# Optimization experiments

Hardware: AMD Instinct MI355X
Metric: run time of the kernel (lower is better)

The kernel has to match this reference:

```python
import jax, jax.numpy as jnp
import numpy as np

N_EMBD = 2048
N_HEAD = 16
HEAD_DIM = N_EMBD // N_HEAD
BATCH = 2
SEQ = 2048


def setup_inputs() -> dict:
    key = jax.random.key(0)
    k1, k2, k3 = jax.random.split(key, 3)
    scale = 0.02
    return {
        "hidden_states": jax.random.normal(k1, (BATCH, SEQ, N_EMBD), dtype=jnp.float32),
        "c_attn_w": jax.random.normal(k2, (N_EMBD, 3 * N_EMBD), dtype=jnp.float32) * scale,
        "c_attn_b": jnp.zeros((3 * N_EMBD,), dtype=jnp.float32),
        "c_proj_w": jax.random.normal(k3, (N_EMBD, N_EMBD), dtype=jnp.float32) * scale,
        "c_proj_b": jnp.zeros((N_EMBD,), dtype=jnp.float32),
    }


def reference(hidden_states, c_attn_w, c_attn_b, c_proj_w, c_proj_b):
    B, S, E = hidden_states.shape
    # Fused QKV projection (Conv1D: x @ W + b)
    qkv = hidden_states @ c_attn_w + c_attn_b  # [B, S, 3E]
    q, k, v = jnp.split(qkv, 3, axis=-1)
    # split heads -> [B, H, S, D]
    def split_heads(t):
        return t.reshape(B, S, N_HEAD, HEAD_DIM).transpose(0, 2, 1, 3)
    q, k, v = split_heads(q), split_heads(k), split_heads(v)
    # scaled scores, causal mask, softmax (dropout p=0 -> identity)
    scores = jnp.einsum("bhqd,bhkd->bhqk", q, k) / jnp.asarray(
        HEAD_DIM ** 0.5, dtype=q.dtype)
    causal = jnp.tril(jnp.ones((S, S), dtype=bool))  # [S, S]
    mask_value = jnp.finfo(scores.dtype).min
    scores = jnp.where(causal[None, None, :, :], scores, mask_value)
    attn = jax.nn.softmax(scores, axis=-1)
    out = jnp.einsum("bhqk,bhkd->bhqd", attn, v)  # [B, H, S, D]
    # merge heads -> [B, S, E]
    out = out.transpose(0, 2, 1, 3).reshape(B, S, E)
    # output projection
    return out @ c_proj_w + c_proj_b
```

## Files before the change

kernel.cpp:

```cpp
#include <hip/hip_runtime.h>
#include <hip/hip_bf16.h>

typedef __bf16 bf16x8 __attribute__((ext_vector_type(8)));
typedef float f32x4 __attribute__((ext_vector_type(4)));

__device__ __forceinline__ float bf2f(unsigned short u) {
  union { unsigned int i; float f; } v; v.i = ((unsigned int)u) << 16; return v.f;
}
__device__ __forceinline__ unsigned short f2bf(float f) {
  union { unsigned int i; float f; } v; v.f = f;
  unsigned int i = v.i;
  return (unsigned short)((i + 0x7FFFu + ((i >> 16) & 1u)) >> 16);
}

typedef const __attribute__((address_space(1))) unsigned int* gas_ptr;
typedef __attribute__((address_space(3))) unsigned int* las_ptr;
__device__ __forceinline__ void gload_lds16(const unsigned short* g, unsigned short* l) {
  __builtin_amdgcn_global_load_lds((gas_ptr)(const void*)g, (las_ptr)(void*)l, 16, 0, 0);
}

__global__ __launch_bounds__(256) void detect_k(const unsigned short* __restrict__ h,
                                                int* __restrict__ flag) {
  __shared__ int s[256];
  int cnt = 0;
  for (int i = threadIdx.x; i < 4096; i += 256) {
    unsigned short u = h[2 * i];
    int e = (u >> 7) & 0xFF;
    if ((e >= 96 && e <= 140) || u == 0) cnt++;
  }
  s[threadIdx.x] = cnt;
  __syncthreads();
  for (int o = 128; o > 0; o >>= 1) {
    if (threadIdx.x < o) s[threadIdx.x] += s[threadIdx.x + o];
    __syncthreads();
  }
  if (threadIdx.x == 0) *flag = (s[0] >= 3600) ? 1 : 0;
}

__global__ __launch_bounds__(256) void cvt_hidden_k(const void* __restrict__ src,
                                                    unsigned short* __restrict__ dst, int n,
                                                    const int* __restrict__ flag) {
  if (*flag) return;
  for (int i = blockIdx.x * 256 + threadIdx.x; i < n; i += gridDim.x * 256)
    dst[i] = f2bf(((const float*)src)[i]);
}

__global__ __launch_bounds__(256) void transpose_w2_k(const void* __restrict__ w_qkv,
                                                      const void* __restrict__ w_proj,
                                                      unsigned short* __restrict__ dst_qkv,
                                                      unsigned short* __restrict__ dst_proj,
                                                      const int* __restrict__ flag) {
  __shared__ unsigned short tile[32][33];
  const int f = *flag;
  int bid = blockIdx.x;
  const void* src;
  unsigned short* dst;
  int R = 2048, C, cx, cy;
  if (bid < 12288) {
    src = w_qkv; dst = dst_qkv; C = 6144; cx = bid % 192; cy = bid / 192;
  } else {
    bid -= 12288;
    src = w_proj; dst = dst_proj; C = 2048; cx = bid % 64; cy = bid / 64;
  }
  const int x = threadIdx.x & 31;
  const int y = threadIdx.x >> 5;
  const int r0 = cy * 32, c0 = cx * 32;
#pragma unroll
  for (int i = 0; i < 4; i++) {
    size_t idx = (size_t)(r0 + y + 8 * i) * C + c0 + x;
    tile[y + 8 * i][x] = f ? ((const unsigned short*)src)[idx]
                           : f2bf(((const float*)src)[idx]);
  }
  __syncthreads();
#pragma unroll
  for (int i = 0; i < 4; i++)
    dst[(size_t)(c0 + y + 8 * i) * R + r0 + x] = tile[x][y + 8 * i];
}

__global__ __launch_bounds__(256) void transpose_v_k(const unsigned short* __restrict__ qkv,
                                                     unsigned short* __restrict__ Vt) {
  __shared__ unsigned short tile[32][33];
  const int bh = blockIdx.z;
  const int b = bh >> 4, hh = bh & 15;
  const int s0 = blockIdx.x * 32, d0 = blockIdx.y * 32;
  const int x = threadIdx.x & 31, y = threadIdx.x >> 5;
#pragma unroll
  for (int i = 0; i < 4; i++)
    tile[y + 8 * i][x] =
        qkv[((size_t)b * 2048 + s0 + y + 8 * i) * 6144 + 4096 + hh * 128 + d0 + x];
  __syncthreads();
#pragma unroll
  for (int i = 0; i < 4; i++)
    Vt[((size_t)bh * 128 + d0 + y + 8 * i) * 2048 + s0 + x] = tile[x][y + 8 * i];
}

__global__ __launch_bounds__(256) void gemm_bias_k(const unsigned short* __restrict__ A_bf,
                                                   const unsigned short* __restrict__ A_cvt,
                                                   const unsigned short* __restrict__ Bt,
                                                   const void* __restrict__ bias,
                                                   void* __restrict__ Cout,
                                                   int M, int N, int K,
                                                   const int* __restrict__ flag,
                                                   int final_out) {
  __shared__ __attribute__((aligned(16))) unsigned short As[128][64];
  __shared__ __attribute__((aligned(16))) unsigned short Bs[128][64];
  const int f = *flag;
  const unsigned short* A = f ? A_bf : A_cvt;
  const int t = threadIdx.x;
  const int wave = t >> 6, lane = t & 63;
  const int col = lane & 15, quad = lane >> 4;
  const int wm = wave >> 1, wn = wave & 1;
  const int m0 = blockIdx.y * 128, n0 = blockIdx.x * 128;
  const int srow = lane >> 3;
  const int schunk = ((lane & 7) ^ srow) * 8;
  const int rsw = col & 7;

  const f32x4 fzero = {0.f, 0.f, 0.f, 0.f};
  f32x4 acc[4][4];
#pragma unroll
  for (int i = 0; i < 4; i++)
#pragma unroll
    for (int j = 0; j < 4; j++) acc[i][j] = fzero;

  for (int k0 = 0; k0 < K; k0 += 64) {
    __syncthreads();
#pragma unroll
    for (int c = 0; c < 4; c++) {
      int seg = wave * 4 + c;
      int row = seg * 8 + srow;
      gload_lds16(&A [(size_t)(m0 + row) * K + k0 + schunk], &As[seg * 8][0]);
      gload_lds16(&Bt[(size_t)(n0 + row) * K + k0 + schunk], &Bs[seg * 8][0]);
    }
    __syncthreads();
#pragma unroll
    for (int ks = 0; ks < 2; ks++) {
      bf16x8 af[4], bfr[4];
#pragma unroll
      for (int i = 0; i < 4; i++)
        af[i] = *(const bf16x8*)&As[wm * 64 + i * 16 + col][(((ks << 2) | quad) ^ rsw) * 8];
#pragma unroll
      for (int j = 0; j < 4; j++)
        bfr[j] = *(const bf16x8*)&Bs[wn * 64 + j * 16 + col][(((ks << 2) | quad) ^ rsw) * 8];
#pragma unroll
      for (int i = 0; i < 4; i++)
#pragma unroll
        for (int j = 0; j < 4; j++)
          acc[i][j] = __builtin_amdgcn_mfma_f32_16x16x32_bf16(af[i], bfr[j], acc[i][j], 0, 0, 0);
    }
  }
  const int f32o = final_out ? (f == 0) : 0;
#pragma unroll
  for (int j = 0; j < 4; j++) {
    int n = n0 + wn * 64 + j * 16 + col;
    float bv = f ? bf2f(((const unsigned short*)bias)[n]) : ((const float*)bias)[n];
#pragma unroll
    for (int i = 0; i < 4; i++)
#pragma unroll
      for (int r = 0; r < 4; r++) {
        int m = m0 + wm * 64 + i * 16 + quad * 4 + r;
        float v = acc[i][j][r] + bv;
        if (f32o) ((float*)Cout)[(size_t)m * N + n] = v;
        else      ((unsigned short*)Cout)[(size_t)m * N + n] = f2bf(v);
      }
  }
}

#define ATT_SCALE 0.08838834764831845f
__global__ __launch_bounds__(256) void attn_k(const unsigned short* __restrict__ qkv,
                                              const unsigned short* __restrict__ Vt,
                                              unsigned short* __restrict__ O) {
  __shared__ __attribute__((aligned(16))) unsigned short Ks[64][136];
  __shared__ __attribute__((aligned(16))) unsigned short Vs[128][72];
  __shared__ __attribute__((aligned(16))) unsigned short Ps[4][16][72];
  const int t = threadIdx.x;
  const int wave = t >> 6, lane = t & 63;
  const int col = lane & 15, quad = lane >> 4;
  const int h = blockIdx.y, b = blockIdx.z;
  const size_t base = (size_t)b * 2048 * 6144;
  const size_t vbase = ((size_t)(b * 16 + h)) * 128 * 2048;
  const int hcol = h * 128;

  const int kr = t >> 2;
  const int kc = (t & 3) * 8;
  const int vr = t >> 1;
  const int vc = (t & 1) * 32;

  const f32x4 fzero = {0.f, 0.f, 0.f, 0.f};

  for (int pass = 0; pass < 2; pass++) {
    const int qt = pass ? (int)blockIdx.x : 31 - (int)blockIdx.x;

    bf16x8 qf[4];
    {
      size_t qrow = base + (size_t)(qt * 64 + wave * 16 + col) * 6144 + hcol;
#pragma unroll
      for (int ks = 0; ks < 4; ks++)
        qf[ks] = *(const bf16x8*)&qkv[qrow + ks * 32 + quad * 8];
    }

    f32x4 o[8];
#pragma unroll
    for (int i = 0; i < 8; i++) o[i] = fzero;
    float l_i[4] = {0.f, 0.f, 0.f, 0.f};

    __syncthreads();
    {
      size_t grow = base + (size_t)kr * 6144 + 2048 + hcol;
#pragma unroll
      for (int p = 0; p < 4; p++)
        *(bf16x8*)&Ks[kr][kc + p * 32] = *(const bf16x8*)&qkv[grow + kc + p * 32];
      size_t vrow = vbase + (size_t)vr * 2048;
#pragma unroll
      for (int c = 0; c < 4; c++)
        *(bf16x8*)&Vs[vr][vc + c * 8] = *(const bf16x8*)&Vt[vrow + vc + c * 8];
    }
    __syncthreads();

    for (int kt = 0; kt <= qt; kt++) {
      bf16x8 kreg[4], vreg[4];
      const bool pf = (kt < qt);
      if (pf) {
        size_t grow = base + (size_t)((kt + 1) * 64 + kr) * 6144 + 2048 + hcol;
#pragma unroll
        for (int p = 0; p < 4; p++)
          kreg[p] = *(const bf16x8*)&qkv[grow + kc + p * 32];
        size_t vrow = vbase + (size_t)vr * 2048 + (kt + 1) * 64;
#pragma unroll
        for (int c = 0; c < 4; c++)
          vreg[c] = *(const bf16x8*)&Vt[vrow + vc + c * 8];
      }

      f32x4 sc[4];
#pragma unroll
      for (int nb = 0; nb < 4; nb++) {
        f32x4 s = fzero;
#pragma unroll
        for (int ks = 0; ks < 4; ks++) {
          bf16x8 kf = *(const bf16x8*)&Ks[nb * 16 + col][ks * 32 + quad * 8];
          s = __builtin_amdgcn_mfma_f32_16x16x32_bf16(qf[ks], kf, s, 0, 0, 0);
        }
        sc[nb] = s;
      }

      const bool diag = (kt == qt);
#pragma unroll
      for (int nb = 0; nb < 4; nb++) {
        int kl = nb * 16 + col;
#pragma unroll
        for (int r = 0; r < 4; r++) {
          float s = sc[nb][r];
          if (diag && kl > wave * 16 + quad * 4 + r) s = -1e30f;
          float p = __expf(s * ATT_SCALE);
          l_i[r] += p;
          Ps[wave][quad * 4 + r][nb * 16 + col] = f2bf(p);
        }
      }
      bf16x8 pfr[2];
#pragma unroll
      for (int ks2 = 0; ks2 < 2; ks2++)
        pfr[ks2] = *(const bf16x8*)&Ps[wave][col][ks2 * 32 + quad * 8];
#pragma unroll
      for (int nbo = 0; nbo < 8; nbo++)
#pragma unroll
        for (int ks2 = 0; ks2 < 2; ks2++) {
          bf16x8 vf = *(const bf16x8*)&Vs[nbo * 16 + col][ks2 * 32 + quad * 8];
          o[nbo] = __builtin_amdgcn_mfma_f32_16x16x32_bf16(pfr[ks2], vf, o[nbo], 0, 0, 0);
        }

      __syncthreads();
      if (pf) {
#pragma unroll
        for (int p = 0; p < 4; p++)
          *(bf16x8*)&Ks[kr][kc + p * 32] = kreg[p];
#pragma unroll
        for (int c = 0; c < 4; c++)
          *(bf16x8*)&Vs[vr][vc + c * 8] = vreg[c];
      }
      __syncthreads();
    }

#pragma unroll
    for (int r = 0; r < 4; r++) {
#pragma unroll
      for (int off = 1; off < 16; off <<= 1)
        l_i[r] += __shfl_xor(l_i[r], off, 64);
      l_i[r] = 1.0f / l_i[r];
    }

#pragma unroll
    for (int nbo = 0; nbo < 8; nbo++)
#pragma unroll
      for (int r = 0; r < 4; r++) {
        int m = qt * 64 + wave * 16 + quad * 4 + r;
        O[((size_t)b * 2048 + m) * 2048 + hcol + nbo * 16 + col] = f2bf(o[nbo][r] * l_i[r]);
      }
  }
}

extern "C" void kernel_launch(void* const* d_in, const int* in_sizes, int n_in,
                              void* d_out, int out_size, void* d_ws, size_t ws_size,
                              hipStream_t stream) {
  (void)in_sizes; (void)n_in; (void)out_size; (void)ws_size;
  int* flag = (int*)d_ws;
  unsigned short* wsu = (unsigned short*)d_ws + 128;
  unsigned short* Wt_qkv    = wsu;
  unsigned short* Wt_proj   = Wt_qkv + (size_t)6144 * 2048;
  unsigned short* QKV       = Wt_proj + (size_t)2048 * 2048;
  unsigned short* hidden_bf = QKV + (size_t)4096 * 6144;
  unsigned short* Obuf      = Wt_qkv;
  unsigned short* Vt        = hidden_bf + (size_t)4096 * 2048;

  detect_k<<<1, 256, 0, stream>>>((const unsigned short*)d_in[0], flag);
  cvt_hidden_k<<<2048, 256, 0, stream>>>(d_in[0], hidden_bf, 4096 * 2048, flag);
  transpose_w2_k<<<16384, 256, 0, stream>>>(d_in[1], d_in[3], Wt_qkv, Wt_proj, flag);
  gemm_bias_k<<<dim3(48, 32), 256, 0, stream>>>((const unsigned short*)d_in[0], hidden_bf,
                                                Wt_qkv, d_in[2], QKV,
                                                4096, 6144, 2048, flag, 0);
  transpose_v_k<<<dim3(64, 4, 32), 256, 0, stream>>>(QKV, Vt);
  attn_k<<<dim3(16, 16, 2), 256, 0, stream>>>(QKV, Vt, Obuf);
  gemm_bias_k<<<dim3(16, 32), 256, 0, stream>>>(Obuf, Obuf, Wt_proj, d_in[4], d_out,
                                                4096, 2048, 2048, flag, 1);
}
```

Before: 417.4 us.

## Fuse prologue kernels and write transposed V from QKV GEMM epilogue

Merges dtype detection, hidden-state conversion and weight transposes into one prologue kernel. Each block recomputes the detection flag locally, so the separate detection launch and its serialization go away. The QKV GEMM now writes V tiles transposed straight into Vt through shared memory, which removes the separate transpose_v kernel and its extra global read and write. Attention switches __expf to exp2f with a prescaled log2(e) constant; this adds some per-block redundant sampling and epilogue syncs in exchange.

```diff
diff --git a/kernel.cpp b/kernel.cpp
--- a/kernel.cpp
+++ b/kernel.cpp
@@ -19,51 +19,45 @@
   __builtin_amdgcn_global_load_lds((gas_ptr)(const void*)g, (las_ptr)(void*)l, 16, 0, 0);
 }
 
-__global__ __launch_bounds__(256) void detect_k(const unsigned short* __restrict__ h,
-                                                int* __restrict__ flag) {
-  __shared__ int s[256];
-  int cnt = 0;
-  for (int i = threadIdx.x; i < 4096; i += 256) {
-    unsigned short u = h[2 * i];
-    int e = (u >> 7) & 0xFF;
-    if ((e >= 96 && e <= 140) || u == 0) cnt++;
-  }
-  s[threadIdx.x] = cnt;
+__global__ __launch_bounds__(256) void prologue_k(const void* __restrict__ hidden,
+                                                  const void* __restrict__ w_qkv,
+                                                  const void* __restrict__ w_proj,
+                                                  unsigned short* __restrict__ hidden_bf,
+                                                  unsigned short* __restrict__ Wt_qkv,
+                                                  unsigned short* __restrict__ Wt_proj,
+                                                  int* __restrict__ flag) {
+  __shared__ unsigned short tile[32][33];
+  __shared__ int s4[4];
+  const int t = threadIdx.x;
+  {
+    const unsigned short* h = (const unsigned short*)hidden;
+    int cnt = 0;
+    for (int i = t; i < 2048; i += 256) {
+      unsigned short u = h[2 * i];
+      int e = (u >> 7) & 0xFF;
+      cnt += ((e >= 96 && e <= 140) || u == 0) ? 1 : 0;
+    }
+#pragma unroll
+    for (int off = 1; off < 64; off <<= 1) cnt += __shfl_xor(cnt, off, 64);
+    if ((t & 63) == 0) s4[t >> 6] = cnt;
+  }
   __syncthreads();
-  for (int o = 128; o > 0; o >>= 1) {
-    if (threadIdx.x < o) s[threadIdx.x] += s[threadIdx.x + o];
-    __syncthreads();
-  }
-  if (threadIdx.x == 0) *flag = (s[0] >= 3600) ? 1 : 0;
-}
-
-__global__ __launch_bounds__(256) void cvt_hidden_k(const void* __restrict__ src,
-                                                    unsigned short* __restrict__ dst, int n,
-                                                    const int* __restrict__ flag) {
-  if (*flag) return;
-  for (int i = blockIdx.x * 256 + threadIdx.x; i < n; i += gridDim.x * 256)
-    dst[i] = f2bf(((const float*)src)[i]);
-}
-
-__global__ __launch_bounds__(256) void transpose_w2_k(const void* __restrict__ w_qkv,
-                                                      const void* __restrict__ w_proj,
-                                                      unsigned short* __restrict__ dst_qkv,
-                                                      unsigned short* __restrict__ dst_proj,
-                                                      const int* __restrict__ flag) {
-  __shared__ unsigned short tile[32][33];
-  const int f = *flag;
+  const int f = (s4[0] + s4[1] + s4[2] + s4[3]) >= 1800;
+  if (blockIdx.x == 0 && t == 0) *flag = f;
+
   int bid = blockIdx.x;
-  const void* src;
-  unsigned short* dst;
-  int R = 2048, C, cx, cy;
-  if (bid < 12288) {
-    src = w_qkv; dst = dst_qkv; C = 6144; cx = bid % 192; cy = bid / 192;
-  } else {
-    bid -= 12288;
-    src = w_proj; dst = dst_proj; C = 2048; cx = bid % 64; cy = bid / 64;
-  }
-  const int x = threadIdx.x & 31;
-  const int y = threadIdx.x >> 5;
+  if (bid < 2048) {
+    if (f) return;
+    const float* src = (const float*)hidden;
+    int base = bid * 4096;
+#pragma unroll
+    for (int k = 0; k < 16; k++) hidden_bf[base + t + 256 * k] = f2bf(src[base + t + 256 * k]);
+    return;
+  }
+  const void* src; unsigned short* dst; int C, cx, cy;
+  if (bid < 14336) { bid -= 2048;  src = w_qkv;  dst = Wt_qkv;  C = 6144; cx = bid % 192; cy = bid / 192; }
+  else             { bid -= 14336; src = w_proj; dst = Wt_proj; C = 2048; cx = bid % 64;  cy = bid / 64;  }
+  const int x = t & 31, y = t >> 5;
   const int r0 = cy * 32, c0 = cx * 32;
 #pragma unroll
   for (int i = 0; i < 4; i++) {
@@ -74,24 +68,7 @@
   __syncthreads();
 #pragma unroll
   for (int i = 0; i < 4; i++)
-    dst[(size_t)(c0 + y + 8 * i) * R + r0 + x] = tile[x][y + 8 * i];
-}
-
-__global__ __launch_bounds__(256) void transpose_v_k(const unsigned short* __restrict__ qkv,
-                                                     unsigned short* __restrict__ Vt) {
-  __shared__ unsigned short tile[32][33];
-  const int bh = blockIdx.z;
-  const int b = bh >> 4, hh = bh & 15;
-  const int s0 = blockIdx.x * 32, d0 = blockIdx.y * 32;
-  const int x = threadIdx.x & 31, y = threadIdx.x >> 5;
-#pragma unroll
-  for (int i = 0; i < 4; i++)
-    tile[y + 8 * i][x] =
-        qkv[((size_t)b * 2048 + s0 + y + 8 * i) * 6144 + 4096 + hh * 128 + d0 + x];
-  __syncthreads();
-#pragma unroll
-  for (int i = 0; i < 4; i++)
-    Vt[((size_t)bh * 128 + d0 + y + 8 * i) * 2048 + s0 + x] = tile[x][y + 8 * i];
+    dst[(size_t)(c0 + y + 8 * i) * 2048 + r0 + x] = tile[x][y + 8 * i];
 }
 
 __global__ __launch_bounds__(256) void gemm_bias_k(const unsigned short* __restrict__ A_bf,
@@ -99,11 +76,13 @@
                                                    const unsigned short* __restrict__ Bt,
                                                    const void* __restrict__ bias,
                                                    void* __restrict__ Cout,
+                                                   unsigned short* __restrict__ Vt,
                                                    int M, int N, int K,
                                                    const int* __restrict__ flag,
-                                                   int final_out) {
-  __shared__ __attribute__((aligned(16))) unsigned short As[128][64];
-  __shared__ __attribute__((aligned(16))) unsigned short Bs[128][64];
+                                                   int final_out, int v_fuse) {
+  __shared__ __attribute__((aligned(16))) unsigned short smem[2][128][64];
+#define As smem[0]
+#define Bs smem[1]
   const int f = *flag;
   const unsigned short* A = f ? A_bf : A_cvt;
   const int t = threadIdx.x;
@@ -148,6 +127,36 @@
           acc[i][j] = __builtin_amdgcn_mfma_f32_16x16x32_bf16(af[i], bfr[j], acc[i][j], 0, 0, 0);
     }
   }
+
+  if (v_fuse && n0 >= 4096) {
+    const int bb = m0 >> 11, hh = (n0 - 4096) >> 7, s0k = m0 & 2047;
+    unsigned short* Tr = &smem[0][0][0];
+#pragma unroll
+    for (int half = 0; half < 2; half++) {
+      __syncthreads();
+      if (wn == half) {
+#pragma unroll
+        for (int j = 0; j < 4; j++) {
+          int n = n0 + wn * 64 + j * 16 + col;
+          float bv = f ? bf2f(((const unsigned short*)bias)[n]) : ((const float*)bias)[n];
+          int dloc = j * 16 + col;
+#pragma unroll
+          for (int i = 0; i < 4; i++)
+#pragma unroll
+            for (int r = 0; r < 4; r++)
+              Tr[dloc * 130 + wm * 64 + i * 16 + quad * 4 + r] = f2bf(acc[i][j][r] + bv);
+        }
+      }
+      __syncthreads();
+      const int r2 = t >> 2, seg = (t & 3) * 32;
+      size_t gaddr = (((size_t)(bb * 16 + hh)) * 128 + half * 64 + r2) * 2048 + s0k + seg;
+#pragma unroll
+      for (int c = 0; c < 4; c++)
+        *(bf16x8*)&Vt[gaddr + c * 8] = *(const bf16x8*)&Tr[r2 * 130 + seg + c * 8];
+    }
+    return;
+  }
+
   const int f32o = final_out ? (f == 0) : 0;
 #pragma unroll
   for (int j = 0; j < 4; j++) {
@@ -163,9 +172,11 @@
         else      ((unsigned short*)Cout)[(size_t)m * N + n] = f2bf(v);
       }
   }
-}
-
-#define ATT_SCALE 0.08838834764831845f
+#undef As
+#undef Bs
+}
+
+#define ATT_SCALE_L2E 0.12751743f
 __global__ __launch_bounds__(256) void attn_k(const unsigned short* __restrict__ qkv,
                                               const unsigned short* __restrict__ Vt,
                                               unsigned short* __restrict__ O) {
@@ -250,7 +261,7 @@
         for (int r = 0; r < 4; r++) {
           float s = sc[nb][r];
           if (diag && kl > wave * 16 + quad * 4 + r) s = -1e30f;
-          float p = __expf(s * ATT_SCALE);
+          float p = exp2f(s * ATT_SCALE_L2E);
           l_i[r] += p;
           Ps[wave][quad * 4 + r][nb * 16 + col] = f2bf(p);
         }
@@ -307,17 +318,15 @@
   unsigned short* Wt_proj   = Wt_qkv + (size_t)6144 * 2048;
   unsigned short* QKV       = Wt_proj + (size_t)2048 * 2048;
   unsigned short* hidden_bf = QKV + (size_t)4096 * 6144;
+  unsigned short* Vt        = hidden_bf + (size_t)4096 * 2048;
   unsigned short* Obuf      = Wt_qkv;
-  unsigned short* Vt        = hidden_bf + (size_t)4096 * 2048;
-
-  detect_k<<<1, 256, 0, stream>>>((const unsigned short*)d_in[0], flag);
-  cvt_hidden_k<<<2048, 256, 0, stream>>>(d_in[0], hidden_bf, 4096 * 2048, flag);
-  transpose_w2_k<<<16384, 256, 0, stream>>>(d_in[1], d_in[3], Wt_qkv, Wt_proj, flag);
+
+  prologue_k<<<18432, 256, 0, stream>>>(d_in[0], d_in[1], d_in[3],
+                                        hidden_bf, Wt_qkv, Wt_proj, flag);
   gemm_bias_k<<<dim3(48, 32), 256, 0, stream>>>((const unsigned short*)d_in[0], hidden_bf,
-                                                Wt_qkv, d_in[2], QKV,
-                                                4096, 6144, 2048, flag, 0);
-  transpose_v_k<<<dim3(64, 4, 32), 256, 0, stream>>>(QKV, Vt);
+                                                Wt_qkv, d_in[2], QKV, Vt,
+                                                4096, 6144, 2048, flag, 0, 1);
   attn_k<<<dim3(16, 16, 2), 256, 0, stream>>>(QKV, Vt, Obuf);
-  gemm_bias_k<<<dim3(16, 32), 256, 0, stream>>>(Obuf, Obuf, Wt_proj, d_in[4], d_out,
-                                                4096, 2048, 2048, flag, 1);
-}
+  gemm_bias_k<<<dim3(16, 32), 256, 0, stream>>>(Obuf, Obuf, Wt_proj, d_in[4], d_out, Vt,
+                                                4096, 2048, 2048, flag, 1, 0);
+}
```

After: 439.5 us. 1.05x slower.
